# Kernel tuning notes

Measured on AMD Instinct MI355X. Metric: run time of the kernel, lower is better.

## Reference

```python
import jax, jax.numpy as jnp
import numpy as np

N_HEADS = 16

def setup_inputs() -> dict:
    key = jax.random.key(0)
    k1, k2, k3 = jax.random.split(key, 3)
    B, T, C = 2, 2048, 1024
    x = jax.random.normal(k1, (B, T, C), dtype=jnp.float32)
    # torch Linear(n_embed, 3*n_embed, bias=False) -> store as [in, out]
    W_qkv = jax.random.normal(k2, (C, 3 * C), dtype=jnp.float32) * (1.0 / np.sqrt(C))
    W_proj = jax.random.normal(k3, (C, C), dtype=jnp.float32) * (1.0 / np.sqrt(C))
    return {"x": x, "W_qkv": W_qkv, "W_proj": W_proj}

def reference(x, W_qkv, W_proj):
    B, T, C = x.shape
    H = N_HEADS
    d = C // H
    qkv = x @ W_qkv                                   # [B, T, 3C]
    q, k, v = jnp.split(qkv, 3, axis=-1)
    # [B, T, C] -> [B, H, T, d]
    q = q.reshape(B, T, H, d).transpose(0, 2, 1, 3)
    k = k.reshape(B, T, H, d).transpose(0, 2, 1, 3)
    v = v.reshape(B, T, H, d).transpose(0, 2, 1, 3)
    scale = 1.0 / np.sqrt(d).astype(np.float32)
    wei = jnp.einsum('bhqd,bhkd->bhqk', q, k) * scale  # [B, H, T, T]
    causal = jnp.tril(jnp.ones((T, T), dtype=bool))
    wei = jnp.where(causal[None, None, :, :], wei, jnp.float32(-jnp.inf))
    wei = jax.nn.softmax(wei, axis=-1)
    out = jnp.einsum('bhqk,bhkd->bhqd', wei, v)        # [B, H, T, d]
    out = out.transpose(0, 2, 1, 3).reshape(B, T, C)
    return out @ W_proj
```

## Files before the change

kernel.cpp:

```cpp
#include <hip/hip_runtime.h>
#include <stdint.h>

typedef __attribute__((ext_vector_type(8))) short short8v;
typedef __attribute__((ext_vector_type(4))) float float4v;
typedef __attribute__((ext_vector_type(4))) unsigned short ushort4v;
typedef __attribute__((ext_vector_type(2))) unsigned int uint2v;
typedef __attribute__((ext_vector_type(4))) unsigned int uint4v;

#define B_SZ 2
#define T_SEQ 2048
#define C_EMB 1024
#define NH 16
#define DH 64
#define M_ROWS (B_SZ * T_SEQ)
#define CEXP 0.18033688f
#define MSHIFT 16.0f
#define MASKVAL -3e30f

__device__ __forceinline__ unsigned short f2bf(float f) {
    unsigned int u = __float_as_uint(f);
    u += 0x7FFFu + ((u >> 16) & 1u);
    return (unsigned short)(u >> 16);
}

__device__ __forceinline__ unsigned int cvtpk_bf16(float lo, float hi) {
    unsigned int r;
    asm("v_cvt_pk_bf16_f32 %0, %1, %2" : "=v"(r) : "v"(lo), "v"(hi));
    return r;
}

__device__ __forceinline__ void gload_lds16(const void* g, void* s) {
    __builtin_amdgcn_global_load_lds(
        (const __attribute__((address_space(1))) void*)g,
        (__attribute__((address_space(3))) void*)s, 16, 0, 0);
}

__device__ __forceinline__ void memfence_sched() { asm volatile("" ::: "memory"); }

__device__ __forceinline__ void block_barrier() {
    memfence_sched();
    __builtin_amdgcn_s_barrier();
    memfence_sched();
}

__global__ __launch_bounds__(256) void k_prep(const float* __restrict__ x,
                                              unsigned short* __restrict__ xb,
                                              const float* __restrict__ Wqkv,
                                              unsigned short* __restrict__ wqkvT,
                                              const float* __restrict__ Wproj,
                                              unsigned short* __restrict__ wprojT) {
    __shared__ float tile[64][65];
    int bid = blockIdx.x;
    if (bid < 4096) {
        int i = bid * 256 + threadIdx.x;
        float4v v = ((const float4v*)x)[i];
        ushort4v o;
        o.x = f2bf(v.x); o.y = f2bf(v.y); o.z = f2bf(v.z); o.w = f2bf(v.w);
        ((ushort4v*)xb)[i] = o;
        return;
    }
    bid -= 4096;
    const float* in;
    unsigned short* out;
    int R, C, cb, rb;
    if (bid < 768) { in = Wqkv; out = wqkvT; R = 1024; C = 3072; cb = bid % 48; rb = bid / 48; }
    else { bid -= 768; in = Wproj; out = wprojT; R = 1024; C = 1024; cb = bid & 15; rb = bid >> 4; }
    const int c0 = cb * 64, r0 = rb * 64;
#pragma unroll
    for (int i = 0; i < 16; ++i) {
        int e = i * 256 + threadIdx.x;
        int r = e >> 6, c = e & 63;
        tile[r][c] = in[(size_t)(r0 + r) * C + c0 + c];
    }
    __syncthreads();
#pragma unroll
    for (int i = 0; i < 16; ++i) {
        int e = i * 256 + threadIdx.x;
        int r = e >> 6, c = e & 63;
        out[(size_t)(c0 + r) * R + r0 + c] = f2bf(tile[c][r]);
    }
}

template<int BM>
__global__ __launch_bounds__(256) void k_gemm_bt(const unsigned short* __restrict__ A,
                                                 const unsigned short* __restrict__ Bt,
                                                 void* __restrict__ Cout,
                                                 unsigned short* __restrict__ vt,
                                                 int M, int N, int K, int mode) {
    constexpr int MI = BM / 32;
    constexpr int ABUF = BM * 32;
    constexpr int SMSZ = 3 * ABUF + 12288;
    __shared__ __align__(16) unsigned short SM[SMSZ];
    unsigned short* As = SM;
    unsigned short* Bs = SM + 3 * ABUF;

    const int tid = threadIdx.x;
    const int lane = tid & 63;
    const int w = tid >> 6;
    const int lr = lane & 15;
    const int lg = lane >> 4;
    const int wr = (w >> 1) * (MI * 16);
    const int wc = (w & 1) * 64;

    const int gx = gridDim.x;
    const int nwg = gx * gridDim.y;
    const int lin = blockIdx.y * gx + blockIdx.x;
    const int q8 = nwg >> 3;
    const int wg = (lin & 7) * q8 + (lin >> 3);
    const int mb = wg / gx;
    const int nb = wg - mb * gx;
    const int m0 = mb * BM;
    const int n0 = nb * 128;

    const unsigned short* aptr = A + (size_t)(m0 + (tid >> 2)) * K + (tid & 3) * 8;
    const unsigned short* bptr = Bt + (size_t)(n0 + (tid >> 2)) * K + (tid & 3) * 8;

    float4v acc[MI][4];
#pragma unroll
    for (int i = 0; i < MI; ++i)
#pragma unroll
        for (int j = 0; j < 4; ++j) acc[i][j] = (float4v){0.f, 0.f, 0.f, 0.f};

#define G_STAGE(buf, t)                                                              \
    do {                                                                             \
        const int k0_ = (t) * 32;                                                    \
        gload_lds16(aptr + k0_, &As[(buf) * ABUF + tid * 8]);                        \
        if constexpr (BM == 128)                                                     \
            gload_lds16(aptr + (size_t)64 * K + k0_, &As[(buf) * ABUF + 2048 + tid * 8]); \
        gload_lds16(bptr + k0_, &Bs[(buf) * 4096 + tid * 8]);                        \
        gload_lds16(bptr + (size_t)64 * K + k0_, &Bs[(buf) * 4096 + 2048 + tid * 8]);\
    } while (0)

    const int NT = K >> 5;
    G_STAGE(0, 0);
    G_STAGE(1, 1);

    int cur = 0;
    for (int t = 0; t < NT; ++t) {
        if (t < NT - 1) {
            if constexpr (BM == 128) { asm volatile("s_waitcnt vmcnt(4)" ::: "memory"); }
            else                     { asm volatile("s_waitcnt vmcnt(3)" ::: "memory"); }
        } else {
            asm volatile("s_waitcnt vmcnt(0)" ::: "memory");
        }
        block_barrier();
        if (t + 2 < NT) { G_STAGE((cur == 0 ? 2 : cur - 1), t + 2); }

        short8v af[MI], bf[4];
#pragma unroll
        for (int i = 0; i < MI; ++i)
            af[i] = *(const short8v*)&As[cur * ABUF + (wr + i * 16 + lr) * 32 + lg * 8];
#pragma unroll
        for (int i = 0; i < 4; ++i)
            bf[i] = *(const short8v*)&Bs[cur * 4096 + (wc + i * 16 + lr) * 32 + lg * 8];
        __builtin_amdgcn_s_setprio(1);
#pragma unroll
        for (int mi = 0; mi < MI; ++mi)
#pragma unroll
            for (int ni = 0; ni < 4; ++ni)
                acc[mi][ni] = __builtin_amdgcn_mfma_f32_16x16x32_bf16(af[mi], bf[ni],
                                                                      acc[mi][ni], 0, 0, 0);
        __builtin_amdgcn_s_setprio(0);
        cur = (cur == 2) ? 0 : cur + 1;
    }
#undef G_STAGE

    if (mode == 2) {
        if constexpr (BM == 128) {
            const int CLD = 132;
            __syncthreads();
            if (n0 < 2 * C_EMB) {
#pragma unroll
                for (int mi = 0; mi < 4; ++mi)
#pragma unroll
                    for (int ni = 0; ni < 4; ++ni)
#pragma unroll
                        for (int r = 0; r < 4; ++r)
                            SM[(wr + mi * 16 + lg * 4 + r) * CLD + wc + ni * 16 + lr] =
                                f2bf(acc[mi][ni][r]);
                __syncthreads();
                unsigned short* Cb = (unsigned short*)Cout;
#pragma unroll
                for (int it = 0; it < 8; ++it) {
                    const int e = it * 2048 + tid * 8;
                    const int r = e >> 7, c = e & 127;
                    short8v v = *(const short8v*)&SM[r * CLD + c];
                    *(short8v*)&Cb[(size_t)(m0 + r) * N + n0 + c] = v;
                }
            } else {
#pragma unroll
                for (int mi = 0; mi < 4; ++mi) {
                    const int rloc = wr + mi * 16 + lg * 4;
                    const int tp = (rloc & ~31) + 8 * ((rloc >> 2) & 3) + 4 * ((rloc >> 4) & 1);
#pragma unroll
                    for (int ni = 0; ni < 4; ++ni) {
                        const int frow = wc + ni * 16 + lr;
                        uint2v uu;
                        uu.x = cvtpk_bf16(acc[mi][ni][0], acc[mi][ni][1]);
                        uu.y = cvtpk_bf16(acc[mi][ni][2], acc[mi][ni][3]);
                        *(uint2v*)&SM[frow * CLD + tp] = uu;
                    }
                }
                __syncthreads();
#pragma unroll
                for (int it = 0; it < 8; ++it) {
                    const int e = it * 2048 + tid * 8;
                    const int f = e >> 7, tt = e & 127;
                    short8v v = *(const short8v*)&SM[f * CLD + tt];
                    const int fg = n0 - 2 * C_EMB + f;
                    const int bh = ((m0 >> 11) << 4) + (fg >> 6);
                    *(short8v*)&vt[(size_t)(bh * DH + (fg & 63)) * T_SEQ + (m0 & (T_SEQ - 1)) + tt] = v;
                }
            }
        }
        return;
    }

#pragma unroll
    for (int mi = 0; mi < MI; ++mi) {
#pragma unroll
        for (int ni = 0; ni < 4; ++ni) {
            int row = m0 + wr + mi * 16 + lg * 4;
            int col = n0 + wc + ni * 16 + lr;
            float* Cf = (float*)Cout;
#pragma unroll
            for (int r = 0; r < 4; ++r) Cf[(size_t)(row + r) * N + col] = acc[mi][ni][r];
        }
    }
}

template<bool MASK>
__device__ __forceinline__ void attn_tile(const unsigned short* __restrict__ Ksb,
                                          const unsigned short* __restrict__ Vsb,
                                          const short8v (&qa)[2][2], short8v ones,
                                          float4v (&o)[2][4], float4v (&accl)[2],
                                          int lr, int lg, int kw, int qw) {
    const int swz = lr & 7;
    short8v kb0[2], kb1[2];
#pragma unroll
    for (int si = 0; si < 2; ++si) {
        const unsigned short* rowp = Ksb + (((2 * kw + si) * 16) + lr) * 64;
        kb0[si] = *(const short8v*)&rowp[(lg ^ swz) * 8];
        kb1[si] = *(const short8v*)&rowp[((4 + lg) ^ swz) * 8];
    }
    float4v s[2][2];
    __builtin_amdgcn_s_setprio(1);
#pragma unroll
    for (int g = 0; g < 2; ++g)
#pragma unroll
        for (int si = 0; si < 2; ++si) {
            float4v acc = (float4v){0.f, 0.f, 0.f, 0.f};
            acc = __builtin_amdgcn_mfma_f32_16x16x32_bf16(kb0[si], qa[g][0], acc, 0, 0, 0);
            acc = __builtin_amdgcn_mfma_f32_16x16x32_bf16(kb1[si], qa[g][1], acc, 0, 0, 0);
            s[g][si] = acc;
        }
    __builtin_amdgcn_s_setprio(0);
    if (MASK) {
#pragma unroll
        for (int g = 0; g < 2; ++g)
#pragma unroll
            for (int si = 0; si < 2; ++si)
#pragma unroll
                for (int r = 0; r < 4; ++r)
                    s[g][si][r] = ((2 * kw + si) * 16 + lg * 4 + r <= (2 * qw + g) * 16 + lr)
                                      ? s[g][si][r] : MASKVAL;
    }

    uint4v pbu[2];
#pragma unroll
    for (int g = 0; g < 2; ++g) {
        float p0[4], p1[4];
#pragma unroll
        for (int r = 0; r < 4; ++r) {
            p0[r] = exp2f(__builtin_fmaf(s[g][0][r], CEXP, -MSHIFT));
            p1[r] = exp2f(__builtin_fmaf(s[g][1][r], CEXP, -MSHIFT));
        }
        pbu[g].x = cvtpk_bf16(p0[0], p0[1]);
        pbu[g].y = cvtpk_bf16(p0[2], p0[3]);
        pbu[g].z = cvtpk_bf16(p1[0], p1[1]);
        pbu[g].w = cvtpk_bf16(p1[2], p1[3]);
    }

    short8v pb0 = *(short8v*)&pbu[0];
    short8v pb1 = *(short8v*)&pbu[1];
    __builtin_amdgcn_s_setprio(1);
    accl[0] = __builtin_amdgcn_mfma_f32_16x16x32_bf16(ones, pb0, accl[0], 0, 0, 0);
    accl[1] = __builtin_amdgcn_mfma_f32_16x16x32_bf16(ones, pb1, accl[1], 0, 0, 0);
#pragma unroll
    for (int n = 0; n < 4; ++n) {
        short8v vb = *(const short8v*)&Vsb[(n * 16 + lr) * 64 + ((kw * 4 + lg) ^ swz) * 8];
        o[0][n] = __builtin_amdgcn_mfma_f32_16x16x32_bf16(vb, pb0, o[0][n], 0, 0, 0);
        o[1][n] = __builtin_amdgcn_mfma_f32_16x16x32_bf16(vb, pb1, o[1][n], 0, 0, 0);
    }
    __builtin_amdgcn_s_setprio(0);
}

__global__ __launch_bounds__(256, 4) void k_attn(const unsigned short* __restrict__ qkv,
                                                 const unsigned short* __restrict__ vt,
                                                 unsigned short* __restrict__ aout) {
    __shared__ __align__(16) unsigned short KV[2][2][64 * 64];

    const int tid = threadIdx.x;
    const int lane = tid & 63;
    const int w = tid >> 6;
    const int lr = lane & 15;
    const int lg = lane >> 4;
    const int kw = w & 1;
    const int qw = w >> 1;

    const int lin = blockIdx.x;
    const int bh = lin & 31;
    const int a = lin >> 5;
    const int j = a & 7, r4 = a >> 3;
    const int qb = (r4 == 0) ? (31 - j) : (r4 == 1) ? (16 + j) : (r4 == 2) ? (15 - j) : j;
    const int q0 = qb * 64;
    const int b = bh >> 4, h = bh & 15;

    short8v qa[2][2];
#pragma unroll
    for (int g = 0; g < 2; ++g) {
        const unsigned short* qrowp =
            qkv + (size_t)(b * T_SEQ + q0 + (2 * qw + g) * 16 + lr) * (3 * C_EMB) + h * DH + lg * 8;
        qa[g][0] = *(const short8v*)qrowp;
        qa[g][1] = *(const short8v*)(qrowp + 32);
    }
    short8v ones;
#pragma unroll
    for (int i = 0; i < 8; ++i) ones[i] = (short)0x3F80;

    float4v o[2][4];
    float4v accl[2] = {(float4v){0.f, 0.f, 0.f, 0.f}, (float4v){0.f, 0.f, 0.f, 0.f}};
#pragma unroll
    for (int g = 0; g < 2; ++g)
#pragma unroll
        for (int n = 0; n < 4; ++n) o[g][n] = (float4v){0.f, 0.f, 0.f, 0.f};

    const int lc = ((tid & 7) ^ ((tid >> 3) & 7)) * 8;
    const unsigned short* kptr =
        qkv + (size_t)(b * T_SEQ + (tid >> 3)) * (3 * C_EMB) + C_EMB + h * DH + lc;
    const unsigned short* vptr = vt + (size_t)(bh * DH + (tid >> 3)) * T_SEQ + lc;

    const int nt = qb + 1;

#define A_STAGE(buf)                                                     \
    do {                                                                 \
        gload_lds16(kptr, &KV[buf][0][tid * 8]);                         \
        gload_lds16(kptr + (size_t)32 * 3 * C_EMB, &KV[buf][0][2048 + tid * 8]); \
        gload_lds16(vptr, &KV[buf][1][tid * 8]);                         \
        gload_lds16(vptr + (size_t)32 * T_SEQ, &KV[buf][1][2048 + tid * 8]);     \
        kptr += 64 * 3 * C_EMB;                                          \
        vptr += 64;                                                      \
    } while (0)

    A_STAGE(0);

    int cur = 0;
    for (int t = 0; t < nt - 1; ++t) {
        A_STAGE(cur ^ 1);
        asm volatile("s_waitcnt vmcnt(4)" ::: "memory");
        block_barrier();
        attn_tile<false>(&KV[cur][0][0], &KV[cur][1][0], qa, ones, o, accl, lr, lg, kw, qw);
        block_barrier();
        cur ^= 1;
    }
    asm volatile("s_waitcnt vmcnt(0)" ::: "memory");
    block_barrier();
    attn_tile<true>(&KV[cur][0][0], &KV[cur][1][0], qa, ones, o, accl, lr, lg, kw, qw);
#undef A_STAGE

    float lt[2] = {accl[0][0], accl[1][0]};
    __syncthreads();
    float* scr = (float*)&KV[0][0][0];
    float* mlp = scr + 6000;
    const int SROW = 68;
    if (kw == 1) {
#pragma unroll
        for (int g = 0; g < 2; ++g)
#pragma unroll
            for (int n = 0; n < 4; ++n)
                *(float4v*)&scr[(qw * 32 + g * 16 + lr) * SROW + n * 16 + 4 * lg] = o[g][n];
        if (lg == 0) {
#pragma unroll
            for (int g = 0; g < 2; ++g) mlp[qw * 32 + g * 16 + lr] = lt[g];
        }
    }
    __syncthreads();
    if (kw == 0) {
#pragma unroll
        for (int g = 0; g < 2; ++g) {
            const float rl = 1.0f / (lt[g] + mlp[qw * 32 + g * 16 + lr]);
            const int trow = b * T_SEQ + q0 + (2 * qw + g) * 16 + lr;
#pragma unroll
            for (int n = 0; n < 4; ++n) {
                float4v o1 = *(float4v*)&scr[(qw * 32 + g * 16 + lr) * SROW + n * 16 + 4 * lg];
                float4v om = o[g][n] + o1;
                uint2v uu;
                uu.x = cvtpk_bf16(om[0] * rl, om[1] * rl);
                uu.y = cvtpk_bf16(om[2] * rl, om[3] * rl);
                *(uint2v*)&aout[(size_t)trow * C_EMB + h * DH + n * 16 + lg * 4] = uu;
            }
        }
    }
}

extern "C" void kernel_launch(void* const* d_in, const int* in_sizes, int n_in,
                              void* d_out, int out_size, void* d_ws, size_t ws_size,
                              hipStream_t stream) {
    const float* x = (const float*)d_in[0];
    const float* Wqkv = (const float*)d_in[1];
    const float* Wproj = (const float*)d_in[2];
    float* out = (float*)d_out;

    unsigned short* xb     = (unsigned short*)d_ws;
    unsigned short* wqkvT  = xb + (size_t)M_ROWS * C_EMB;
    unsigned short* wprojT = wqkvT + (size_t)3 * C_EMB * C_EMB;
    unsigned short* qkvb   = wprojT + (size_t)C_EMB * C_EMB;
    unsigned short* vtb    = qkvb + (size_t)M_ROWS * 3 * C_EMB;
    unsigned short* attb   = vtb + (size_t)M_ROWS * C_EMB;

    k_prep<<<4096 + 768 + 256, 256, 0, stream>>>(x, xb, Wqkv, wqkvT, Wproj, wprojT);
    k_gemm_bt<128><<<dim3(3 * C_EMB / 128, M_ROWS / 128), 256, 0, stream>>>(
        xb, wqkvT, (void*)qkvb, vtb, M_ROWS, 3 * C_EMB, C_EMB, 2);
    k_attn<<<dim3(B_SZ * NH * T_SEQ / 64), 256, 0, stream>>>(qkvb, vtb, attb);
    k_gemm_bt<64><<<dim3(C_EMB / 128, M_ROWS / 64), 256, 0, stream>>>(
        attb, wprojT, (void*)out, nullptr, M_ROWS, C_EMB, C_EMB, 1);
}
```

Baseline: 94.33 us.

## Triple-buffer K tiles and drop the second barrier per attention iteration

Splits the shared K/V staging buffer into a three-slot K ring and a two-slot V ring. K is prefetched two tiles ahead and V one tile ahead. The rotation lets each loop iteration use a single block barrier instead of two, cutting synchronisation stalls in the causal attention loop. LDS use per block grows from 32KB to 40KB, which may pressure the 4-blocks-per-CU occupancy target. The vmcnt(4) wait still forces the next K tile to land, so the effective K prefetch depth stays shallow.

```diff
diff --git a/kernel.cpp b/kernel.cpp
--- a/kernel.cpp
+++ b/kernel.cpp
@@ -298,7 +298,8 @@
 __global__ __launch_bounds__(256, 4) void k_attn(const unsigned short* __restrict__ qkv,
                                                  const unsigned short* __restrict__ vt,
                                                  unsigned short* __restrict__ aout) {
-    __shared__ __align__(16) unsigned short KV[2][2][64 * 64];
+    __shared__ __align__(16) unsigned short Ks[3][64 * 64];
+    __shared__ __align__(16) unsigned short Vs[2][64 * 64];
 
     const int tid = threadIdx.x;
     const int lane = tid & 63;
@@ -342,35 +343,46 @@
 
     const int nt = qb + 1;
 
-#define A_STAGE(buf)                                                     \
-    do {                                                                 \
-        gload_lds16(kptr, &KV[buf][0][tid * 8]);                         \
-        gload_lds16(kptr + (size_t)32 * 3 * C_EMB, &KV[buf][0][2048 + tid * 8]); \
-        gload_lds16(vptr, &KV[buf][1][tid * 8]);                         \
-        gload_lds16(vptr + (size_t)32 * T_SEQ, &KV[buf][1][2048 + tid * 8]);     \
-        kptr += 64 * 3 * C_EMB;                                          \
-        vptr += 64;                                                      \
+#define K_STAGE(buf)                                                              \
+    do {                                                                          \
+        gload_lds16(kptr, &Ks[buf][tid * 8]);                                     \
+        gload_lds16(kptr + (size_t)32 * 3 * C_EMB, &Ks[buf][2048 + tid * 8]);     \
+        kptr += 64 * 3 * C_EMB;                                                   \
     } while (0)
-
-    A_STAGE(0);
-
-    int cur = 0;
-    for (int t = 0; t < nt - 1; ++t) {
-        A_STAGE(cur ^ 1);
-        asm volatile("s_waitcnt vmcnt(4)" ::: "memory");
+#define V_STAGE(buf)                                                              \
+    do {                                                                          \
+        gload_lds16(vptr, &Vs[buf][tid * 8]);                                     \
+        gload_lds16(vptr + (size_t)32 * T_SEQ, &Vs[buf][2048 + tid * 8]);         \
+        vptr += 64;                                                               \
+    } while (0)
+
+    K_STAGE(0);
+    V_STAGE(0);
+    if (nt > 1) K_STAGE(1);
+
+    int kc = 0, vc = 0;
+    for (int t = 0; t < nt; ++t) {
         block_barrier();
-        attn_tile<false>(&KV[cur][0][0], &KV[cur][1][0], qa, ones, o, accl, lr, lg, kw, qw);
-        block_barrier();
-        cur ^= 1;
-    }
-    asm volatile("s_waitcnt vmcnt(0)" ::: "memory");
-    block_barrier();
-    attn_tile<true>(&KV[cur][0][0], &KV[cur][1][0], qa, ones, o, accl, lr, lg, kw, qw);
-#undef A_STAGE
+        const bool hasK2 = (t + 2 < nt);
+        const bool hasV1 = (t + 1 < nt);
+        if (hasK2) K_STAGE((kc + 2 > 2) ? kc - 1 : kc + 2);
+        if (hasV1) V_STAGE(vc ^ 1);
+        if (hasK2)       { asm volatile("s_waitcnt vmcnt(4)" ::: "memory"); }
+        else if (hasV1)  { asm volatile("s_waitcnt vmcnt(2)" ::: "memory"); }
+        else             { asm volatile("s_waitcnt vmcnt(0)" ::: "memory"); }
+        if (t < nt - 1)
+            attn_tile<false>(&Ks[kc][0], &Vs[vc][0], qa, ones, o, accl, lr, lg, kw, qw);
+        else
+            attn_tile<true>(&Ks[kc][0], &Vs[vc][0], qa, ones, o, accl, lr, lg, kw, qw);
+        kc = (kc == 2) ? 0 : kc + 1;
+        vc ^= 1;
+    }
+#undef K_STAGE
+#undef V_STAGE
 
     float lt[2] = {accl[0][0], accl[1][0]};
     __syncthreads();
-    float* scr = (float*)&KV[0][0][0];
+    float* scr = (float*)&Ks[0][0];
     float* mlp = scr + 6000;
     const int SROW = 68;
     if (kw == 1) {
```

After: 100.7 us. 1.07x slower.
